# Performance work log

Measured on AMD Instinct MI355X. Metric: run time of the kernel, lower is better.

Reference implementation:

```python
import jax, jax.numpy as jnp
import numpy as np

N = 100000
E = 3200000
F_IN, H1, H2, C = 512, 32, 16, 11


def setup_inputs() -> dict:
    key = jax.random.key(0)
    ks = jax.random.split(key, 8)
    x = jax.random.normal(ks[0], (N, F_IN), dtype=jnp.float32)
    edge_index = jax.random.randint(ks[1], (2, E), 0, N, dtype=jnp.int64)
    def glorot(k, fan_in, fan_out):
        lim = np.sqrt(6.0 / (fan_in + fan_out)).astype(np.float32)
        return jax.random.uniform(k, (fan_in, fan_out), jnp.float32, -lim, lim)
    return {
        "x": x,
        "edge_index": edge_index,
        "W1": glorot(ks[2], F_IN, H1), "b1": jnp.zeros((H1,), jnp.float32),
        "W2": glorot(ks[3], H1, H2),   "b2": jnp.zeros((H2,), jnp.float32),
        "W3": glorot(ks[4], H2, C),    "b3": jnp.zeros((C,), jnp.float32),
    }


def _gcn_conv(x, W, b, src, dst, deg_inv_sqrt):
    # GCNConv: D^{-1/2}(A+I)D^{-1/2} X W + b, self-loops handled analytically.
    h = x @ W                                   # [N, out]
    norm = deg_inv_sqrt[src] * deg_inv_sqrt[dst]  # [E]
    msg = h[src] * norm[:, None]                # gather + scale
    agg = jax.ops.segment_sum(msg, dst, num_segments=x.shape[0])
    agg = agg + h * (deg_inv_sqrt ** 2)[:, None]  # self-loop term
    return agg + b


def reference(x, edge_index, W1, b1, W2, b2, W3, b3):
    src, dst = edge_index[0], edge_index[1]
    n = x.shape[0]
    # degree with self-loops, counted on destination (PyG convention)
    deg = jax.ops.segment_sum(jnp.ones((dst.shape[0],), x.dtype), dst, num_segments=n) + 1.0
    deg_inv_sqrt = jax.lax.rsqrt(deg)
    h = jax.nn.relu(_gcn_conv(x, W1, b1, src, dst, deg_inv_sqrt))
    # F.dropout(training=self.training) is identity in eval mode
    h = jax.nn.relu(_gcn_conv(h, W2, b2, src, dst, deg_inv_sqrt))
    h = _gcn_conv(h, W3, b3, src, dst, deg_inv_sqrt)
    return jax.nn.log_softmax(h, axis=1)
```

## Files before the change

### kernel.cpp

```cpp
#include <hip/hip_runtime.h>

static __device__ __forceinline__ unsigned short f2bf(float f) {
    unsigned u = __float_as_uint(f);
    unsigned r = (u + 0x7FFF + ((u >> 16) & 1)) >> 16;
    return (unsigned short)r;
}
static __device__ __forceinline__ float bf2f(unsigned short h) {
    return __uint_as_float(((unsigned)h) << 16);
}

typedef __attribute__((ext_vector_type(8))) short bf16x8;
typedef __attribute__((ext_vector_type(4))) float f32x4;

#define BKT_SHIFT 7
#define BKT_NODES 128
#define CHUNK 32768

__global__ __launch_bounds__(512) void hist_k(const int* __restrict__ dst, int* __restrict__ histG,
                                              int B, int NB, int E) {
    __shared__ int hist[1024];
    int tid = threadIdx.x;
    for (int i = tid; i < NB; i += 512) hist[i] = 0;
    __syncthreads();
    int base = blockIdx.x * CHUNK;
    for (int i = tid; i < CHUNK; i += 512) {
        int e = base + i;
        if (e >= E) break;
        atomicAdd(&hist[dst[e] >> BKT_SHIFT], 1);
    }
    __syncthreads();
    for (int i = tid; i < NB; i += 512) histG[(size_t)i * B + blockIdx.x] = hist[i];
}

__global__ __launch_bounds__(512) void scatter_k(const int* __restrict__ src, const int* __restrict__ dst,
                                                 const int* __restrict__ scanG, int* __restrict__ pairs,
                                                 int B, int NB, int E) {
    __shared__ int sbase[1024];
    __shared__ int scnt[1024];
    int tid = threadIdx.x;
    for (int i = tid; i < NB; i += 512) {
        sbase[i] = scanG[(size_t)i * B + blockIdx.x];
        scnt[i] = 0;
    }
    __syncthreads();
    int base = blockIdx.x * CHUNK;
    for (int i = tid; i < CHUNK; i += 512) {
        int e = base + i;
        if (e >= E) break;
        int d = dst[e], s = src[e];
        int b = d >> BKT_SHIFT;
        int r = atomicAdd(&scnt[b], 1);
        pairs[sbase[b] + r] = (s << BKT_SHIFT) | (d & (BKT_NODES - 1));
    }
}

#define SCAN_VPT 8
#define SCAN_ELEMS 2048

__global__ __launch_bounds__(256) void scan1(const int* __restrict__ in, int* __restrict__ out,
                                             int* __restrict__ blksum, int n) {
    __shared__ int sh[256];
    int base = blockIdx.x * SCAN_ELEMS + threadIdx.x * SCAN_VPT;
    int v[SCAN_VPT];
    int sum = 0;
    #pragma unroll
    for (int j = 0; j < SCAN_VPT; ++j) {
        v[j] = (base + j < n) ? in[base + j] : 0;
        sum += v[j];
    }
    sh[threadIdx.x] = sum;
    __syncthreads();
    for (int off = 1; off < 256; off <<= 1) {
        int t = (threadIdx.x >= off) ? sh[threadIdx.x - off] : 0;
        __syncthreads();
        sh[threadIdx.x] += t;
        __syncthreads();
    }
    if (threadIdx.x == 255) blksum[blockIdx.x] = sh[255];
    int run = sh[threadIdx.x] - sum;
    #pragma unroll
    for (int j = 0; j < SCAN_VPT; ++j) {
        if (base + j < n) out[base + j] = run;
        run += v[j];
    }
}

__global__ __launch_bounds__(256) void scan2(int* __restrict__ blksum, int nb) {
    __shared__ int sh[256];
    int t = threadIdx.x;
    int v = (t < nb) ? blksum[t] : 0;
    sh[t] = v;
    __syncthreads();
    for (int off = 1; off < 256; off <<= 1) {
        int u = (t >= off) ? sh[t - off] : 0;
        __syncthreads();
        sh[t] += u;
        __syncthreads();
    }
    if (t < nb) blksum[t] = sh[t] - v;
}

__global__ void scan3(int* __restrict__ out, const int* __restrict__ blksum, int n) {
    int i = blockIdx.x * blockDim.x + threadIdx.x;
    if (i < n) out[i] += blksum[i >> 11];
}

#define SORT_CAP 8192

__global__ __launch_bounds__(512) void sort_bucket(const int* __restrict__ pairs,
        const int* __restrict__ scanG, int B, int NB,
        int* __restrict__ csr_src, int* __restrict__ node_start,
        int* __restrict__ cnt, float* __restrict__ dis, int n, int E) {
    __shared__ int keys[SORT_CAP];
    __shared__ int lcnt[BKT_NODES];
    __shared__ int lscan[BKT_NODES];
    __shared__ int lfill[BKT_NODES];
    int bkt = blockIdx.x, tid = threadIdx.x;
    int e0 = scanG[(size_t)bkt * B];
    int e1 = (bkt + 1 < NB) ? scanG[(size_t)(bkt + 1) * B] : E;
    int m = e1 - e0;
    if (tid < BKT_NODES) { lcnt[tid] = 0; lfill[tid] = 0; }
    __syncthreads();
    for (int i = tid; i < m; i += 512) {
        int k = pairs[e0 + i];
        if (i < SORT_CAP) keys[i] = k;
        atomicAdd(&lcnt[k & (BKT_NODES - 1)], 1);
    }
    __syncthreads();
    if (tid == 0) {
        int run = 0;
        for (int i = 0; i < BKT_NODES; ++i) { lscan[i] = run; run += lcnt[i]; }
    }
    __syncthreads();
    int nb0 = bkt << BKT_SHIFT;
    if (tid < BKT_NODES && nb0 + tid < n) {
        int deg = lcnt[tid];
        node_start[nb0 + tid] = e0 + lscan[tid];
        cnt[nb0 + tid] = deg;
        dis[nb0 + tid] = rsqrtf((float)deg + 1.0f);
    }
    for (int i = tid; i < m; i += 512) {
        int k = (i < SORT_CAP) ? keys[i] : pairs[e0 + i];
        int d = k & (BKT_NODES - 1);
        int pos = lscan[d] + atomicAdd(&lfill[d], 1);
        csr_src[e0 + pos] = k >> BKT_SHIFT;
    }
}


__global__ __launch_bounds__(256) void gemm1_mfma(const float* __restrict__ x, const float* __restrict__ W,
                                                  const float* __restrict__ dis, unsigned short* __restrict__ g, int n) {
    __shared__ __attribute__((aligned(16))) unsigned short wT[32][520];
    __shared__ __attribute__((aligned(16))) unsigned short xb[64][72];
    int tid = threadIdx.x;
    int node0 = blockIdx.x * 64;

    #pragma unroll
    for (int r = 0; r < 16; ++r) {
        int fi = tid + r * 256;
        int k = fi >> 3, c4 = (fi & 7) * 4;
        float4 wv = *(const float4*)(W + (size_t)k * 32 + c4);
        wT[c4 + 0][k] = f2bf(wv.x);
        wT[c4 + 1][k] = f2bf(wv.y);
        wT[c4 + 2][k] = f2bf(wv.z);
        wT[c4 + 3][k] = f2bf(wv.w);
    }

    int wv_ = tid >> 6;
    int lane = tid & 63;
    int mrow = lane & 15;
    int kg = lane >> 4;
    f32x4 acc0 = {0.f, 0.f, 0.f, 0.f};
    f32x4 acc1 = {0.f, 0.f, 0.f, 0.f};

    for (int k0 = 0; k0 < 512; k0 += 64) {
        __syncthreads();
        #pragma unroll
        for (int r = 0; r < 4; ++r) {
            int fi = tid + r * 256;
            int nd = fi >> 4, kq = (fi & 15) * 4;
            int gn = min(node0 + nd, n - 1);
            float4 xv = *(const float4*)(x + (size_t)gn * 512 + k0 + kq);
            ushort4 p;
            p.x = f2bf(xv.x); p.y = f2bf(xv.y); p.z = f2bf(xv.z); p.w = f2bf(xv.w);
            *(ushort4*)(&xb[nd][kq]) = p;
        }
        __syncthreads();
        #pragma unroll
        for (int ks = 0; ks < 2; ++ks) {
            bf16x8 a  = *(const bf16x8*)(&xb[wv_ * 16 + mrow][ks * 32 + kg * 8]);
            bf16x8 b0 = *(const bf16x8*)(&wT[mrow][k0 + ks * 32 + kg * 8]);
            bf16x8 b1 = *(const bf16x8*)(&wT[16 + mrow][k0 + ks * 32 + kg * 8]);
            acc0 = __builtin_amdgcn_mfma_f32_16x16x32_bf16(a, b0, acc0, 0, 0, 0);
            acc1 = __builtin_amdgcn_mfma_f32_16x16x32_bf16(a, b1, acc1, 0, 0, 0);
        }
    }
    #pragma unroll
    for (int j = 0; j < 4; ++j) {
        int node = node0 + wv_ * 16 + kg * 4 + j;
        if (node < n) {
            float dv = dis[node];
            g[(size_t)node * 32 + mrow]      = f2bf(acc0[j] * dv);
            g[(size_t)node * 32 + 16 + mrow] = f2bf(acc1[j] * dv);
        }
    }
}


__global__ __launch_bounds__(256) void gather1(const int* __restrict__ csr_src,
        const int* __restrict__ start, const int* __restrict__ cnt,
        const unsigned short* __restrict__ g1, const float* __restrict__ dis,
        const float* __restrict__ b1, const float* __restrict__ W2,
        unsigned short* __restrict__ g2, int n) {
    __shared__ float w2s[32 * 16];
    for (int i = threadIdx.x; i < 512; i += 256) w2s[i] = W2[i];
    __syncthreads();
    int node = blockIdx.x * 4 + (threadIdx.x >> 6);
    if (node >= n) return;
    int lane = threadIdx.x & 63;
    int f = lane & 31;
    int j = lane >> 5;
    int i0 = start[node], i1 = i0 + cnt[node];
    float acc = 0.f;
    int i = i0 + j;
    for (; i + 6 < i1; i += 8) {
        int s1 = csr_src[i];
        int s2 = csr_src[i + 2];
        int s3 = csr_src[i + 4];
        int s4 = csr_src[i + 6];
        unsigned short v1 = g1[(size_t)s1 * 32 + f];
        unsigned short v2 = g1[(size_t)s2 * 32 + f];
        unsigned short v3 = g1[(size_t)s3 * 32 + f];
        unsigned short v4 = g1[(size_t)s4 * 32 + f];
        acc += bf2f(v1) + bf2f(v2) + bf2f(v3) + bf2f(v4);
    }
    for (; i < i1; i += 2) acc += bf2f(g1[(size_t)csr_src[i] * 32 + f]);
    acc += __shfl_xor(acc, 32);
    float dv = dis[node];
    float val = (acc + bf2f(g1[(size_t)node * 32 + f])) * dv + b1[f];
    val = fmaxf(val, 0.f);
    int c = lane & 15;
    int kh = (lane >> 4) & 1;
    float p = 0.f;
    #pragma unroll
    for (int kk = 0; kk < 16; ++kk) {
        int k = kh * 16 + kk;
        float xk = __shfl(val, k);
        p = fmaf(xk, w2s[k * 16 + c], p);
    }
    p += __shfl_xor(p, 16);
    if (lane < 16) g2[(size_t)node * 16 + c] = f2bf(p * dv);
}


__global__ __launch_bounds__(256) void gather2(const int* __restrict__ csr_src,
        const int* __restrict__ start, const int* __restrict__ cnt,
        const unsigned short* __restrict__ g2, const float* __restrict__ dis,
        const float* __restrict__ b2, const float* __restrict__ W3,
        unsigned short* __restrict__ g3, int n) {
    __shared__ float w3s[16 * 16];
    if (threadIdx.x < 256) {
        int k = threadIdx.x >> 4, c = threadIdx.x & 15;
        w3s[threadIdx.x] = (c < 11) ? W3[(size_t)k * 11 + c] : 0.f;
    }
    __syncthreads();
    int node = blockIdx.x * 4 + (threadIdx.x >> 6);
    if (node >= n) return;
    int lane = threadIdx.x & 63;
    int f = lane & 15;
    int j = lane >> 4;
    int i0 = start[node], i1 = i0 + cnt[node];
    float acc = 0.f;
    int i = i0 + j;
    for (; i + 12 < i1; i += 16) {
        int s1 = csr_src[i];
        int s2 = csr_src[i + 4];
        int s3 = csr_src[i + 8];
        int s4 = csr_src[i + 12];
        unsigned short v1 = g2[(size_t)s1 * 16 + f];
        unsigned short v2 = g2[(size_t)s2 * 16 + f];
        unsigned short v3 = g2[(size_t)s3 * 16 + f];
        unsigned short v4 = g2[(size_t)s4 * 16 + f];
        acc += bf2f(v1) + bf2f(v2) + bf2f(v3) + bf2f(v4);
    }
    for (; i < i1; i += 4) acc += bf2f(g2[(size_t)csr_src[i] * 16 + f]);
    acc += __shfl_xor(acc, 16);
    acc += __shfl_xor(acc, 32);
    float dv = dis[node];
    float val = (acc + bf2f(g2[(size_t)node * 16 + f])) * dv + b2[f];
    val = fmaxf(val, 0.f);
    int c = lane & 15;
    int kq = lane >> 4;
    float p = 0.f;
    #pragma unroll
    for (int kk = 0; kk < 4; ++kk) {
        int k = kq * 4 + kk;
        float xk = __shfl(val, k);
        p = fmaf(xk, w3s[k * 16 + c], p);
    }
    p += __shfl_xor(p, 16);
    p += __shfl_xor(p, 32);
    if (lane < 16) g3[(size_t)node * 16 + c] = f2bf(p * dv);
}


__global__ __launch_bounds__(256) void gather3(const int* __restrict__ csr_src,
        const int* __restrict__ start, const int* __restrict__ cnt,
        const unsigned short* __restrict__ g, const float* __restrict__ dis,
        const float* __restrict__ bias, float* __restrict__ out, int n) {
    int node = blockIdx.x * 4 + (threadIdx.x >> 6);
    if (node >= n) return;
    int lane = threadIdx.x & 63;
    int f = lane & 15;
    int j = lane >> 4;
    int i0 = start[node], i1 = i0 + cnt[node];
    float acc = 0.f;
    int i = i0 + j;
    for (; i + 12 < i1; i += 16) {
        int s1 = csr_src[i];
        int s2 = csr_src[i + 4];
        int s3 = csr_src[i + 8];
        int s4 = csr_src[i + 12];
        unsigned short v1 = g[(size_t)s1 * 16 + f];
        unsigned short v2 = g[(size_t)s2 * 16 + f];
        unsigned short v3 = g[(size_t)s3 * 16 + f];
        unsigned short v4 = g[(size_t)s4 * 16 + f];
        acc += bf2f(v1) + bf2f(v2) + bf2f(v3) + bf2f(v4);
    }
    for (; i < i1; i += 4) acc += bf2f(g[(size_t)csr_src[i] * 16 + f]);
    acc += __shfl_xor(acc, 16);
    acc += __shfl_xor(acc, 32);
    float val = (acc + bf2f(g[(size_t)node * 16 + f])) * dis[node] + ((f < 11) ? bias[f] : 0.f);
    float vm = (f < 11) ? val : -3.0e38f;
    #pragma unroll
    for (int m = 1; m < 16; m <<= 1) vm = fmaxf(vm, __shfl_xor(vm, m));
    float ex = (f < 11) ? __expf(val - vm) : 0.f;
    float sum = ex;
    #pragma unroll
    for (int m = 1; m < 16; m <<= 1) sum += __shfl_xor(sum, m);
    if (lane < 11) out[(size_t)node * 11 + f] = val - (__logf(sum) + vm);
}


extern "C" void kernel_launch(void* const* d_in, const int* in_sizes, int n_in,
                              void* d_out, int out_size, void* d_ws, size_t ws_size,
                              hipStream_t stream) {
    const float* x  = (const float*)d_in[0];
    const int*   ei = (const int*)d_in[1];
    const float* W1 = (const float*)d_in[2];
    const float* b1 = (const float*)d_in[3];
    const float* W2 = (const float*)d_in[4];
    const float* b2 = (const float*)d_in[5];
    const float* W3 = (const float*)d_in[6];
    const float* b3 = (const float*)d_in[7];
    float* out = (float*)d_out;

    const int n = in_sizes[0] / 512;
    const int E = in_sizes[1] / 2;
    const int* src = ei;
    const int* dst = ei + E;

    const int NB = (n + BKT_NODES - 1) >> BKT_SHIFT;
    const int B  = (E + CHUNK - 1) / CHUNK;
    const int NBB = NB * B;
    const int nb_scan = (NBB + SCAN_ELEMS - 1) / SCAN_ELEMS;

    int* ws0 = (int*)d_ws;
    size_t off = 0;
    int*   cnt     = ws0 + off; off += (size_t)n;
    float* dis     = (float*)(ws0 + off); off += (size_t)n;
    int*   nstart  = ws0 + off; off += (size_t)n;
    int*   scanG   = ws0 + off; off += (size_t)NBB;
    int*   blksum  = ws0 + off; off += 256;
    int*   pairs   = ws0 + off; off += (size_t)E;
    int*   csr_src = ws0 + off; off += (size_t)E;
    unsigned short* g1 = (unsigned short*)(ws0 + off); off += (size_t)n * 16;
    unsigned short* g2 = (unsigned short*)(ws0 + off); off += (size_t)n * 8;
    unsigned short* g3 = (unsigned short*)(ws0 + off); off += (size_t)n * 8;
    int*   histG   = (int*)g1;

    hist_k<<<B, 512, 0, stream>>>(dst, histG, B, NB, E);
    scan1<<<nb_scan, 256, 0, stream>>>(histG, scanG, blksum, NBB);
    scan2<<<1, 256, 0, stream>>>(blksum, nb_scan);
    scan3<<<(NBB + 255) / 256, 256, 0, stream>>>(scanG, blksum, NBB);
    scatter_k<<<B, 512, 0, stream>>>(src, dst, scanG, pairs, B, NB, E);
    sort_bucket<<<NB, 512, 0, stream>>>(pairs, scanG, B, NB, csr_src, nstart, cnt, dis, n, E);

    gemm1_mfma<<<(n + 63) / 64, 256, 0, stream>>>(x, W1, dis, g1, n);
    gather1<<<(n + 3) / 4, 256, 0, stream>>>(csr_src, nstart, cnt, g1, dis, b1, W2, g2, n);
    gather2<<<(n + 3) / 4, 256, 0, stream>>>(csr_src, nstart, cnt, g2, dis, b2, W3, g3, n);
    gather3<<<(n + 3) / 4, 256, 0, stream>>>(csr_src, nstart, cnt, g3, dis, b3, out, n);
}
```

Measured before the change: 342.8 us.

## Vectorize gather loads to bf16 pairs, fold scan3 into consumers, pre-convert W1

The gather kernels now load two bf16 features per 32-bit load, so each lane covers a feature pair and more edges run in parallel per wavefront. The reductions and the downstream tiny matmul/softmax are reorganised to match. The scan3 fixup kernel is removed: scatter and sort read scanG plus the block offset directly. W1 is converted to transposed bf16 once by a new small kernel, so each GEMM block copies it with vector loads instead of converting per block. The cost is more shuffle reductions and one extra tiny launch.

```diff
diff --git a/kernel.cpp b/kernel.cpp
--- a/kernel.cpp
+++ b/kernel.cpp
@@ -8,8 +8,11 @@
 static __device__ __forceinline__ float bf2f(unsigned short h) {
     return __uint_as_float(((unsigned)h) << 16);
 }
+static __device__ __forceinline__ float bflo(unsigned v) { return __uint_as_float(v << 16); }
+static __device__ __forceinline__ float bfhi(unsigned v) { return __uint_as_float(v & 0xFFFF0000u); }
 
 typedef __attribute__((ext_vector_type(8))) short bf16x8;
+typedef __attribute__((ext_vector_type(8))) unsigned short u16x8;
 typedef __attribute__((ext_vector_type(4))) float f32x4;
 
 #define BKT_SHIFT 7
@@ -33,13 +36,14 @@
 }
 
 __global__ __launch_bounds__(512) void scatter_k(const int* __restrict__ src, const int* __restrict__ dst,
-                                                 const int* __restrict__ scanG, int* __restrict__ pairs,
-                                                 int B, int NB, int E) {
+                                                 const int* __restrict__ scanG, const int* __restrict__ blksum,
+                                                 int* __restrict__ pairs, int B, int NB, int E) {
     __shared__ int sbase[1024];
     __shared__ int scnt[1024];
     int tid = threadIdx.x;
     for (int i = tid; i < NB; i += 512) {
-        sbase[i] = scanG[(size_t)i * B + blockIdx.x];
+        size_t idx = (size_t)i * B + blockIdx.x;
+        sbase[i] = scanG[idx] + blksum[idx >> 11];
         scnt[i] = 0;
     }
     __syncthreads();
@@ -100,15 +104,18 @@
     if (t < nb) blksum[t] = sh[t] - v;
 }
 
-__global__ void scan3(int* __restrict__ out, const int* __restrict__ blksum, int n) {
-    int i = blockIdx.x * blockDim.x + threadIdx.x;
-    if (i < n) out[i] += blksum[i >> 11];
+__global__ __launch_bounds__(256) void wconv(const float* __restrict__ W, unsigned short* __restrict__ W1T) {
+    int gidx = blockIdx.x * 256 + threadIdx.x;
+    if (gidx < 32 * 512) {
+        int c = gidx >> 9, k = gidx & 511;
+        W1T[gidx] = f2bf(W[(size_t)k * 32 + c]);
+    }
 }
 
 #define SORT_CAP 8192
 
 __global__ __launch_bounds__(512) void sort_bucket(const int* __restrict__ pairs,
-        const int* __restrict__ scanG, int B, int NB,
+        const int* __restrict__ scanG, const int* __restrict__ blksum, int B, int NB,
         int* __restrict__ csr_src, int* __restrict__ node_start,
         int* __restrict__ cnt, float* __restrict__ dis, int n, int E) {
     __shared__ int keys[SORT_CAP];
@@ -116,8 +123,13 @@
     __shared__ int lscan[BKT_NODES];
     __shared__ int lfill[BKT_NODES];
     int bkt = blockIdx.x, tid = threadIdx.x;
-    int e0 = scanG[(size_t)bkt * B];
-    int e1 = (bkt + 1 < NB) ? scanG[(size_t)(bkt + 1) * B] : E;
+    size_t idx0 = (size_t)bkt * B;
+    int e0 = scanG[idx0] + blksum[idx0 >> 11];
+    int e1 = E;
+    if (bkt + 1 < NB) {
+        size_t idx1 = (size_t)(bkt + 1) * B;
+        e1 = scanG[idx1] + blksum[idx1 >> 11];
+    }
     int m = e1 - e0;
     if (tid < BKT_NODES) { lcnt[tid] = 0; lfill[tid] = 0; }
     __syncthreads();
@@ -148,7 +160,7 @@
 }
 
 
-__global__ __launch_bounds__(256) void gemm1_mfma(const float* __restrict__ x, const float* __restrict__ W,
+__global__ __launch_bounds__(256) void gemm1_mfma(const float* __restrict__ x, const unsigned short* __restrict__ W1T,
                                                   const float* __restrict__ dis, unsigned short* __restrict__ g, int n) {
     __shared__ __attribute__((aligned(16))) unsigned short wT[32][520];
     __shared__ __attribute__((aligned(16))) unsigned short xb[64][72];
@@ -156,14 +168,10 @@
     int node0 = blockIdx.x * 64;
 
     #pragma unroll
-    for (int r = 0; r < 16; ++r) {
-        int fi = tid + r * 256;
-        int k = fi >> 3, c4 = (fi & 7) * 4;
-        float4 wv = *(const float4*)(W + (size_t)k * 32 + c4);
-        wT[c4 + 0][k] = f2bf(wv.x);
-        wT[c4 + 1][k] = f2bf(wv.y);
-        wT[c4 + 2][k] = f2bf(wv.z);
-        wT[c4 + 3][k] = f2bf(wv.w);
+    for (int r = 0; r < 8; ++r) {
+        int u8 = tid + r * 256;
+        int c = u8 >> 6, kq = (u8 & 63) * 8;
+        *(u16x8*)(&wT[c][kq]) = *(const u16x8*)(W1T + (size_t)c * 512 + kq);
     }
 
     int wv_ = tid >> 6;
@@ -218,37 +226,45 @@
     int node = blockIdx.x * 4 + (threadIdx.x >> 6);
     if (node >= n) return;
     int lane = threadIdx.x & 63;
-    int f = lane & 31;
-    int j = lane >> 5;
+    int fpair = lane & 15;
+    int j = lane >> 4;
     int i0 = start[node], i1 = i0 + cnt[node];
-    float acc = 0.f;
+    float alo = 0.f, ahi = 0.f;
     int i = i0 + j;
-    for (; i + 6 < i1; i += 8) {
+    for (; i + 12 < i1; i += 16) {
         int s1 = csr_src[i];
-        int s2 = csr_src[i + 2];
-        int s3 = csr_src[i + 4];
-        int s4 = csr_src[i + 6];
-        unsigned short v1 = g1[(size_t)s1 * 32 + f];
-        unsigned short v2 = g1[(size_t)s2 * 32 + f];
-        unsigned short v3 = g1[(size_t)s3 * 32 + f];
-        unsigned short v4 = g1[(size_t)s4 * 32 + f];
-        acc += bf2f(v1) + bf2f(v2) + bf2f(v3) + bf2f(v4);
-    }
-    for (; i < i1; i += 2) acc += bf2f(g1[(size_t)csr_src[i] * 32 + f]);
-    acc += __shfl_xor(acc, 32);
+        int s2 = csr_src[i + 4];
+        int s3 = csr_src[i + 8];
+        int s4 = csr_src[i + 12];
+        unsigned v1 = *(const unsigned*)(g1 + (size_t)s1 * 32 + fpair * 2);
+        unsigned v2 = *(const unsigned*)(g1 + (size_t)s2 * 32 + fpair * 2);
+        unsigned v3 = *(const unsigned*)(g1 + (size_t)s3 * 32 + fpair * 2);
+        unsigned v4 = *(const unsigned*)(g1 + (size_t)s4 * 32 + fpair * 2);
+        alo += bflo(v1) + bflo(v2) + bflo(v3) + bflo(v4);
+        ahi += bfhi(v1) + bfhi(v2) + bfhi(v3) + bfhi(v4);
+    }
+    for (; i < i1; i += 4) {
+        unsigned v = *(const unsigned*)(g1 + (size_t)csr_src[i] * 32 + fpair * 2);
+        alo += bflo(v); ahi += bfhi(v);
+    }
+    alo += __shfl_xor(alo, 16); alo += __shfl_xor(alo, 32);
+    ahi += __shfl_xor(ahi, 16); ahi += __shfl_xor(ahi, 32);
     float dv = dis[node];
-    float val = (acc + bf2f(g1[(size_t)node * 32 + f])) * dv + b1[f];
-    val = fmaxf(val, 0.f);
-    int c = lane & 15;
-    int kh = (lane >> 4) & 1;
+    unsigned sv = *(const unsigned*)(g1 + (size_t)node * 32 + fpair * 2);
+    float vlo = fmaxf((alo + bflo(sv)) * dv + b1[2 * fpair], 0.f);
+    float vhi = fmaxf((ahi + bfhi(sv)) * dv + b1[2 * fpair + 1], 0.f);
+    int c = fpair;
     float p = 0.f;
     #pragma unroll
-    for (int kk = 0; kk < 16; ++kk) {
-        int k = kh * 16 + kk;
-        float xk = __shfl(val, k);
-        p = fmaf(xk, w2s[k * 16 + c], p);
+    for (int qq = 0; qq < 4; ++qq) {
+        int q = j * 4 + qq;
+        float xlo = __shfl(vlo, q);
+        float xhi = __shfl(vhi, q);
+        p = fmaf(xlo, w2s[(2 * q) * 16 + c], p);
+        p = fmaf(xhi, w2s[(2 * q + 1) * 16 + c], p);
     }
     p += __shfl_xor(p, 16);
+    p += __shfl_xor(p, 32);
     if (lane < 16) g2[(size_t)node * 16 + c] = f2bf(p * dv);
 }
 
@@ -267,35 +283,40 @@
     int node = blockIdx.x * 4 + (threadIdx.x >> 6);
     if (node >= n) return;
     int lane = threadIdx.x & 63;
-    int f = lane & 15;
-    int j = lane >> 4;
+    int fpair = lane & 7;
+    int j = lane >> 3;
     int i0 = start[node], i1 = i0 + cnt[node];
-    float acc = 0.f;
+    float alo = 0.f, ahi = 0.f;
     int i = i0 + j;
-    for (; i + 12 < i1; i += 16) {
+    for (; i + 24 < i1; i += 32) {
         int s1 = csr_src[i];
-        int s2 = csr_src[i + 4];
-        int s3 = csr_src[i + 8];
-        int s4 = csr_src[i + 12];
-        unsigned short v1 = g2[(size_t)s1 * 16 + f];
-        unsigned short v2 = g2[(size_t)s2 * 16 + f];
-        unsigned short v3 = g2[(size_t)s3 * 16 + f];
-        unsigned short v4 = g2[(size_t)s4 * 16 + f];
-        acc += bf2f(v1) + bf2f(v2) + bf2f(v3) + bf2f(v4);
-    }
-    for (; i < i1; i += 4) acc += bf2f(g2[(size_t)csr_src[i] * 16 + f]);
-    acc += __shfl_xor(acc, 16);
-    acc += __shfl_xor(acc, 32);
+        int s2 = csr_src[i + 8];
+        int s3 = csr_src[i + 16];
+        int s4 = csr_src[i + 24];
+        unsigned v1 = *(const unsigned*)(g2 + (size_t)s1 * 16 + fpair * 2);
+        unsigned v2 = *(const unsigned*)(g2 + (size_t)s2 * 16 + fpair * 2);
+        unsigned v3 = *(const unsigned*)(g2 + (size_t)s3 * 16 + fpair * 2);
+        unsigned v4 = *(const unsigned*)(g2 + (size_t)s4 * 16 + fpair * 2);
+        alo += bflo(v1) + bflo(v2) + bflo(v3) + bflo(v4);
+        ahi += bfhi(v1) + bfhi(v2) + bfhi(v3) + bfhi(v4);
+    }
+    for (; i < i1; i += 8) {
+        unsigned v = *(const unsigned*)(g2 + (size_t)csr_src[i] * 16 + fpair * 2);
+        alo += bflo(v); ahi += bfhi(v);
+    }
+    alo += __shfl_xor(alo, 8); alo += __shfl_xor(alo, 16); alo += __shfl_xor(alo, 32);
+    ahi += __shfl_xor(ahi, 8); ahi += __shfl_xor(ahi, 16); ahi += __shfl_xor(ahi, 32);
     float dv = dis[node];
-    float val = (acc + bf2f(g2[(size_t)node * 16 + f])) * dv + b2[f];
-    val = fmaxf(val, 0.f);
+    unsigned sv = *(const unsigned*)(g2 + (size_t)node * 16 + fpair * 2);
+    float vlo = fmaxf((alo + bflo(sv)) * dv + b2[2 * fpair], 0.f);
+    float vhi = fmaxf((ahi + bfhi(sv)) * dv + b2[2 * fpair + 1], 0.f);
     int c = lane & 15;
-    int kq = lane >> 4;
+    int j2 = lane >> 4;
     float p = 0.f;
     #pragma unroll
     for (int kk = 0; kk < 4; ++kk) {
-        int k = kq * 4 + kk;
-        float xk = __shfl(val, k);
+        int k = j2 * 4 + kk;
+        float xk = (kk & 1) ? __shfl(vhi, k >> 1) : __shfl(vlo, k >> 1);
         p = fmaf(xk, w3s[k * 16 + c], p);
     }
     p += __shfl_xor(p, 16);
@@ -311,34 +332,46 @@
     int node = blockIdx.x * 4 + (threadIdx.x >> 6);
     if (node >= n) return;
     int lane = threadIdx.x & 63;
-    int f = lane & 15;
-    int j = lane >> 4;
+    int fpair = lane & 7;
+    int j = lane >> 3;
     int i0 = start[node], i1 = i0 + cnt[node];
-    float acc = 0.f;
+    float alo = 0.f, ahi = 0.f;
     int i = i0 + j;
-    for (; i + 12 < i1; i += 16) {
+    for (; i + 24 < i1; i += 32) {
         int s1 = csr_src[i];
-        int s2 = csr_src[i + 4];
-        int s3 = csr_src[i + 8];
-        int s4 = csr_src[i + 12];
-        unsigned short v1 = g[(size_t)s1 * 16 + f];
-        unsigned short v2 = g[(size_t)s2 * 16 + f];
-        unsigned short v3 = g[(size_t)s3 * 16 + f];
-        unsigned short v4 = g[(size_t)s4 * 16 + f];
-        acc += bf2f(v1) + bf2f(v2) + bf2f(v3) + bf2f(v4);
-    }
-    for (; i < i1; i += 4) acc += bf2f(g[(size_t)csr_src[i] * 16 + f]);
-    acc += __shfl_xor(acc, 16);
-    acc += __shfl_xor(acc, 32);
-    float val = (acc + bf2f(g[(size_t)node * 16 + f])) * dis[node] + ((f < 11) ? bias[f] : 0.f);
-    float vm = (f < 11) ? val : -3.0e38f;
-    #pragma unroll
-    for (int m = 1; m < 16; m <<= 1) vm = fmaxf(vm, __shfl_xor(vm, m));
-    float ex = (f < 11) ? __expf(val - vm) : 0.f;
-    float sum = ex;
-    #pragma unroll
-    for (int m = 1; m < 16; m <<= 1) sum += __shfl_xor(sum, m);
-    if (lane < 11) out[(size_t)node * 11 + f] = val - (__logf(sum) + vm);
+        int s2 = csr_src[i + 8];
+        int s3 = csr_src[i + 16];
+        int s4 = csr_src[i + 24];
+        unsigned v1 = *(const unsigned*)(g + (size_t)s1 * 16 + fpair * 2);
+        unsigned v2 = *(const unsigned*)(g + (size_t)s2 * 16 + fpair * 2);
+        unsigned v3 = *(const unsigned*)(g + (size_t)s3 * 16 + fpair * 2);
+        unsigned v4 = *(const unsigned*)(g + (size_t)s4 * 16 + fpair * 2);
+        alo += bflo(v1) + bflo(v2) + bflo(v3) + bflo(v4);
+        ahi += bfhi(v1) + bfhi(v2) + bfhi(v3) + bfhi(v4);
+    }
+    for (; i < i1; i += 8) {
+        unsigned v = *(const unsigned*)(g + (size_t)csr_src[i] * 16 + fpair * 2);
+        alo += bflo(v); ahi += bfhi(v);
+    }
+    alo += __shfl_xor(alo, 8); alo += __shfl_xor(alo, 16); alo += __shfl_xor(alo, 32);
+    ahi += __shfl_xor(ahi, 8); ahi += __shfl_xor(ahi, 16); ahi += __shfl_xor(ahi, 32);
+    unsigned sv = *(const unsigned*)(g + (size_t)node * 16 + fpair * 2);
+    float dvn = dis[node];
+    int flo = 2 * fpair, fhi = 2 * fpair + 1;
+    bool oklo = flo < 11, okhi = fhi < 11;
+    float vlo = (alo + bflo(sv)) * dvn + (oklo ? bias[flo] : 0.f);
+    float vhi = (ahi + bfhi(sv)) * dvn + (okhi ? bias[fhi] : 0.f);
+    float m = fmaxf(oklo ? vlo : -3.0e38f, okhi ? vhi : -3.0e38f);
+    m = fmaxf(m, __shfl_xor(m, 1));
+    m = fmaxf(m, __shfl_xor(m, 2));
+    m = fmaxf(m, __shfl_xor(m, 4));
+    float s = (oklo ? __expf(vlo - m) : 0.f) + (okhi ? __expf(vhi - m) : 0.f);
+    s += __shfl_xor(s, 1); s += __shfl_xor(s, 2); s += __shfl_xor(s, 4);
+    float ls = __logf(s) + m;
+    if (lane < 8) {
+        if (oklo) out[(size_t)node * 11 + flo] = vlo - ls;
+        if (okhi) out[(size_t)node * 11 + fhi] = vhi - ls;
+    }
 }
 
 
@@ -377,16 +410,17 @@
     unsigned short* g1 = (unsigned short*)(ws0 + off); off += (size_t)n * 16;
     unsigned short* g2 = (unsigned short*)(ws0 + off); off += (size_t)n * 8;
     unsigned short* g3 = (unsigned short*)(ws0 + off); off += (size_t)n * 8;
+    unsigned short* W1T = (unsigned short*)(ws0 + off); off += 8192;
     int*   histG   = (int*)g1;
 
     hist_k<<<B, 512, 0, stream>>>(dst, histG, B, NB, E);
     scan1<<<nb_scan, 256, 0, stream>>>(histG, scanG, blksum, NBB);
     scan2<<<1, 256, 0, stream>>>(blksum, nb_scan);
-    scan3<<<(NBB + 255) / 256, 256, 0, stream>>>(scanG, blksum, NBB);
-    scatter_k<<<B, 512, 0, stream>>>(src, dst, scanG, pairs, B, NB, E);
-    sort_bucket<<<NB, 512, 0, stream>>>(pairs, scanG, B, NB, csr_src, nstart, cnt, dis, n, E);
-
-    gemm1_mfma<<<(n + 63) / 64, 256, 0, stream>>>(x, W1, dis, g1, n);
+    wconv<<<64, 256, 0, stream>>>(W1, W1T);
+    scatter_k<<<B, 512, 0, stream>>>(src, dst, scanG, blksum, pairs, B, NB, E);
+    sort_bucket<<<NB, 512, 0, stream>>>(pairs, scanG, blksum, B, NB, csr_src, nstart, cnt, dis, n, E);
+
+    gemm1_mfma<<<(n + 63) / 64, 256, 0, stream>>>(x, W1T, dis, g1, n);
     gather1<<<(n + 3) / 4, 256, 0, stream>>>(csr_src, nstart, cnt, g1, dis, b1, W2, g2, n);
     gather2<<<(n + 3) / 4, 256, 0, stream>>>(csr_src, nstart, cnt, g2, dis, b2, W3, g3, n);
     gather3<<<(n + 3) / 4, 256, 0, stream>>>(csr_src, nstart, cnt, g3, dis, b3, out, n);
```

Measured after the change: 318.8 us. -7.0%, faster.
